# Kernel tuning notes

Measured on AMD Instinct MI355X. Metric: run time of the kernel, lower is better.

Reference implementation:

```python
import jax, jax.numpy as jnp
import numpy as np

BR = 1_000_000
D = 128


def setup_inputs() -> dict:
    key = jax.random.key(0)
    ks = jax.random.split(key, 7)
    return {
        "subject_embeddings": jax.random.normal(ks[0], (BR, D), dtype=jnp.float32),
        "object_embeddings": jax.random.normal(ks[1], (BR, D), dtype=jnp.float32),
        "Vs": jax.random.normal(ks[2], (D, D), dtype=jnp.float32) / np.sqrt(D),
        "Vo": jax.random.normal(ks[3], (D, D), dtype=jnp.float32) / np.sqrt(D),
        "Ws": jax.random.normal(ks[4], (D, D), dtype=jnp.float32) / np.sqrt(D),
        "Wo": jax.random.normal(ks[5], (D, D), dtype=jnp.float32) / np.sqrt(D),
        "w": jax.random.normal(ks[6], (D,), dtype=jnp.float32),
    }


def reference(subject_embeddings, object_embeddings, Vs, Vo, Ws, Wo, w):
    s, o = subject_embeddings, object_embeddings
    # nn.Linear(x) == x @ W.T (no bias)
    gate = jax.nn.sigmoid(s @ Vs.T + o @ Vo.T)               # [Br, d]
    dot_ow = jnp.sum(o * w[None, :], axis=1, keepdims=True)  # [Br, 1]
    interaction = s * dot_ow                                  # [Br, d]
    direction = jax.nn.relu(s @ Ws.T + o @ Wo.T + interaction)
    return gate * direction
```

## Files before the change

### kernel.cpp

```cpp
#include <hip/hip_runtime.h>
#include <hip/hip_bf16.h>

#define BR_N     1000000
#define DIM      128
#define TILE_M   64
#define NTILES   (BR_N / TILE_M)
#define NTHREADS 512
#define NBLOCKS  1024

typedef __attribute__((ext_vector_type(8))) short    bf16x8;
typedef __attribute__((ext_vector_type(4))) float    f32x4;
typedef __attribute__((ext_vector_type(4))) unsigned u32x4;

static __device__ __forceinline__ unsigned pk2(float a, float b) {
    union { __hip_bfloat162 h; unsigned u; } v;
    v.h = __float22bfloat162_rn(float2{a, b});
    return v.u;
}

union FragU { bf16x8 v; u32x4 u; };

static __device__ __forceinline__ bf16x8 cvt8(const f32x4 a, const f32x4 b) {
    FragU r;
    r.u.x = pk2(a.x, a.y);
    r.u.y = pk2(a.z, a.w);
    r.u.z = pk2(b.x, b.y);
    r.u.w = pk2(b.z, b.w);
    return r.v;
}

static __device__ __forceinline__ float bf2f(unsigned short b) {
    union { unsigned u; float f; } v;
    v.u = ((unsigned)b) << 16;
    return v.f;
}

__global__ __launch_bounds__(NTHREADS, 2)
void relup_kernel(const float* __restrict__ S, const float* __restrict__ O,
                  const float* __restrict__ Vs, const float* __restrict__ Vo,
                  const float* __restrict__ Ws, const float* __restrict__ Wo,
                  const float* __restrict__ W1, float* __restrict__ out)
{
    __shared__ __align__(16) unsigned char sT[TILE_M * 256];
    __shared__ __align__(16) unsigned char oT[TILE_M * 256];
    __shared__ float dotv[TILE_M];

    const int tid  = threadIdx.x;
    const int lane = tid & 63;
    const int wv   = tid >> 6;
    const int c0   = wv << 4;

    bf16x8 fVs[4], fVo[4], fWs[4], fWo[4];
    {
        const int wr = c0 + (lane & 15);
        const int wc = (lane >> 4) << 3;
        #pragma unroll
        for (int kk = 0; kk < 4; ++kk) {
            const int off = wr * DIM + kk * 32 + wc;
            fVs[kk] = cvt8(*(const f32x4*)(Vs + off), *(const f32x4*)(Vs + off + 4));
            fVo[kk] = cvt8(*(const f32x4*)(Vo + off), *(const f32x4*)(Vo + off + 4));
            fWs[kk] = cvt8(*(const f32x4*)(Ws + off), *(const f32x4*)(Ws + off + 4));
            fWo[kk] = cvt8(*(const f32x4*)(Wo + off), *(const f32x4*)(Wo + off + 4));
        }
    }

    const int str = tid >> 3;
    const int seg = tid & 7;
    const int swS = (str & 7) << 4;
    const int sb0 = str * 256 + ((seg * 32) ^ swS);
    const int sb1 = str * 256 + (((seg * 32) + 16) ^ swS);
    const float* wp = W1 + seg * 16;

    int t = blockIdx.x;

    f32x4 Ps0, Ps1, Ps2, Ps3, Po0, Po1, Po2, Po3;
    {
        const float* sp = S + (t * TILE_M + str) * DIM + seg * 16;
        const float* op = O + (t * TILE_M + str) * DIM + seg * 16;
        Ps0 = ((const f32x4*)sp)[0]; Ps1 = ((const f32x4*)sp)[1];
        Ps2 = ((const f32x4*)sp)[2]; Ps3 = ((const f32x4*)sp)[3];
        Po0 = ((const f32x4*)op)[0]; Po1 = ((const f32x4*)op)[1];
        Po2 = ((const f32x4*)op)[2]; Po3 = ((const f32x4*)op)[3];
    }

    while (t < NTILES) {
        const int row0 = t * TILE_M;
        const int tn   = t + (int)gridDim.x;
        const int tp   = (tn < NTILES) ? tn : t;

        {
            const f32x4 w0 = ((const f32x4*)wp)[0], w1 = ((const f32x4*)wp)[1];
            const f32x4 w2 = ((const f32x4*)wp)[2], w3 = ((const f32x4*)wp)[3];
            float p = Po0.x*w0.x + Po0.y*w0.y + Po0.z*w0.z + Po0.w*w0.w
                    + Po1.x*w1.x + Po1.y*w1.y + Po1.z*w1.z + Po1.w*w1.w
                    + Po2.x*w2.x + Po2.y*w2.y + Po2.z*w2.z + Po2.w*w2.w
                    + Po3.x*w3.x + Po3.y*w3.y + Po3.z*w3.z + Po3.w*w3.w;

            u32x4 pa = { pk2(Ps0.x,Ps0.y), pk2(Ps0.z,Ps0.w), pk2(Ps1.x,Ps1.y), pk2(Ps1.z,Ps1.w) };
            u32x4 pb = { pk2(Ps2.x,Ps2.y), pk2(Ps2.z,Ps2.w), pk2(Ps3.x,Ps3.y), pk2(Ps3.z,Ps3.w) };
            u32x4 pc = { pk2(Po0.x,Po0.y), pk2(Po0.z,Po0.w), pk2(Po1.x,Po1.y), pk2(Po1.z,Po1.w) };
            u32x4 pd = { pk2(Po2.x,Po2.y), pk2(Po2.z,Po2.w), pk2(Po3.x,Po3.y), pk2(Po3.z,Po3.w) };
            *(u32x4*)(sT + sb0) = pa;
            *(u32x4*)(sT + sb1) = pb;
            *(u32x4*)(oT + sb0) = pc;
            *(u32x4*)(oT + sb1) = pd;

            {
                const float* sp = S + (tp * TILE_M + str) * DIM + seg * 16;
                const float* op = O + (tp * TILE_M + str) * DIM + seg * 16;
                Ps0 = ((const f32x4*)sp)[0]; Ps1 = ((const f32x4*)sp)[1];
                Ps2 = ((const f32x4*)sp)[2]; Ps3 = ((const f32x4*)sp)[3];
                Po0 = ((const f32x4*)op)[0]; Po1 = ((const f32x4*)op)[1];
                Po2 = ((const f32x4*)op)[2]; Po3 = ((const f32x4*)op)[3];
            }

            p += __shfl_xor(p, 1);
            p += __shfl_xor(p, 2);
            p += __shfl_xor(p, 4);
            if (seg == 0) dotv[str] = p;
        }
        __syncthreads();

        #pragma unroll
        for (int b = 0; b < 4; ++b) {
            const int r0  = b << 4;
            const int ar  = r0 + (lane & 15);
            const int swA = (ar & 7) << 4;
            const int acb = (lane >> 4) << 4;
            bf16x8 fs[4], fo[4];
            #pragma unroll
            for (int kk = 0; kk < 4; ++kk) {
                const int cb = ((kk << 6) + acb) ^ swA;
                fs[kk] = *(const bf16x8*)(sT + ar * 256 + cb);
                fo[kk] = *(const bf16x8*)(oT + ar * 256 + cb);
            }
            f32x4 accg = {0.f, 0.f, 0.f, 0.f};
            f32x4 accd = {0.f, 0.f, 0.f, 0.f};
            #pragma unroll
            for (int kk = 0; kk < 4; ++kk) {
                accg = __builtin_amdgcn_mfma_f32_16x16x32_bf16(fs[kk], fVs[kk], accg, 0, 0, 0);
                accg = __builtin_amdgcn_mfma_f32_16x16x32_bf16(fo[kk], fVo[kk], accg, 0, 0, 0);
                accd = __builtin_amdgcn_mfma_f32_16x16x32_bf16(fs[kk], fWs[kk], accd, 0, 0, 0);
                accd = __builtin_amdgcn_mfma_f32_16x16x32_bf16(fo[kk], fWo[kk], accd, 0, 0, 0);
            }
            const int col = c0 + (lane & 15);
            #pragma unroll
            for (int r = 0; r < 4; ++r) {
                const int row = r0 + ((lane >> 4) << 2) + r;
                const int gi  = (row0 + row) * DIM + col;
                const int sOff = row * 256 + ((col * 2) ^ ((row & 7) << 4));
                const float sval  = bf2f(*(const unsigned short*)(sT + sOff));
                const float inter = sval * dotv[row];
                const float gate  = 1.0f / (1.0f + __expf(-accg[r]));
                float dir = accd[r] + inter;
                dir = dir > 0.0f ? dir : 0.0f;
                out[gi] = gate * dir;
            }
        }
        __syncthreads();
        t = tn;
    }
}

extern "C" void kernel_launch(void* const* d_in, const int* in_sizes, int n_in,
                              void* d_out, int out_size, void* d_ws, size_t ws_size,
                              hipStream_t stream) {
    const float* S  = (const float*)d_in[0];
    const float* O  = (const float*)d_in[1];
    const float* Vs = (const float*)d_in[2];
    const float* Vo = (const float*)d_in[3];
    const float* Ws = (const float*)d_in[4];
    const float* Wo = (const float*)d_in[5];
    const float* w  = (const float*)d_in[6];
    float* out = (float*)d_out;
    relup_kernel<<<NBLOCKS, NTHREADS, 0, stream>>>(S, O, Vs, Vo, Ws, Wo, w, out);
}
```

Baseline: 320.8 us.

## Double-buffer LDS tiles and transpose MFMA operands for vectorized output stores

Doubles the shared-memory staging buffers so the next tile's bf16 pack, LDS store and dot-product run after the current tile's MFMA work. This removes one of the two barriers per iteration. The MFMA operand order is swapped so each lane holds four consecutive output columns of a single row, which allows one 16-byte global store per lane instead of four scalar stores. The cost is twice the LDS footprint, which may limit occupancy at two blocks per CU, and the result tile must be rebuilt in the transposed layout.

```diff
diff --git a/kernel.cpp b/kernel.cpp
--- a/kernel.cpp
+++ b/kernel.cpp
@@ -11,6 +11,7 @@
 typedef __attribute__((ext_vector_type(8))) short    bf16x8;
 typedef __attribute__((ext_vector_type(4))) float    f32x4;
 typedef __attribute__((ext_vector_type(4))) unsigned u32x4;
+typedef __attribute__((ext_vector_type(2))) unsigned u32x2;
 
 static __device__ __forceinline__ unsigned pk2(float a, float b) {
     union { __hip_bfloat162 h; unsigned u; } v;
@@ -41,9 +42,9 @@
                   const float* __restrict__ Ws, const float* __restrict__ Wo,
                   const float* __restrict__ W1, float* __restrict__ out)
 {
-    __shared__ __align__(16) unsigned char sT[TILE_M * 256];
-    __shared__ __align__(16) unsigned char oT[TILE_M * 256];
-    __shared__ float dotv[TILE_M];
+    __shared__ __align__(16) unsigned char sT[2][TILE_M * 256];
+    __shared__ __align__(16) unsigned char oT[2][TILE_M * 256];
+    __shared__ float dotv[2][TILE_M];
 
     const int tid  = threadIdx.x;
     const int lane = tid & 63;
@@ -71,7 +72,8 @@
     const int sb1 = str * 256 + (((seg * 32) + 16) ^ swS);
     const float* wp = W1 + seg * 16;
 
-    int t = blockIdx.x;
+    int t   = blockIdx.x;
+    int cur = 0;
 
     f32x4 Ps0, Ps1, Ps2, Ps3, Po0, Po1, Po2, Po3;
     {
@@ -82,45 +84,45 @@
         Po0 = ((const f32x4*)op)[0]; Po1 = ((const f32x4*)op)[1];
         Po2 = ((const f32x4*)op)[2]; Po3 = ((const f32x4*)op)[3];
     }
+    {
+        const f32x4 w0 = ((const f32x4*)wp)[0], w1 = ((const f32x4*)wp)[1];
+        const f32x4 w2 = ((const f32x4*)wp)[2], w3 = ((const f32x4*)wp)[3];
+        float p = Po0.x*w0.x + Po0.y*w0.y + Po0.z*w0.z + Po0.w*w0.w
+                + Po1.x*w1.x + Po1.y*w1.y + Po1.z*w1.z + Po1.w*w1.w
+                + Po2.x*w2.x + Po2.y*w2.y + Po2.z*w2.z + Po2.w*w2.w
+                + Po3.x*w3.x + Po3.y*w3.y + Po3.z*w3.z + Po3.w*w3.w;
+        u32x4 pa = { pk2(Ps0.x,Ps0.y), pk2(Ps0.z,Ps0.w), pk2(Ps1.x,Ps1.y), pk2(Ps1.z,Ps1.w) };
+        u32x4 pb = { pk2(Ps2.x,Ps2.y), pk2(Ps2.z,Ps2.w), pk2(Ps3.x,Ps3.y), pk2(Ps3.z,Ps3.w) };
+        u32x4 pc = { pk2(Po0.x,Po0.y), pk2(Po0.z,Po0.w), pk2(Po1.x,Po1.y), pk2(Po1.z,Po1.w) };
+        u32x4 pd = { pk2(Po2.x,Po2.y), pk2(Po2.z,Po2.w), pk2(Po3.x,Po3.y), pk2(Po3.z,Po3.w) };
+        *(u32x4*)(sT[0] + sb0) = pa;
+        *(u32x4*)(sT[0] + sb1) = pb;
+        *(u32x4*)(oT[0] + sb0) = pc;
+        *(u32x4*)(oT[0] + sb1) = pd;
+        p += __shfl_xor(p, 1);
+        p += __shfl_xor(p, 2);
+        p += __shfl_xor(p, 4);
+        if (seg == 0) dotv[0][str] = p;
+    }
+    __syncthreads();
 
     while (t < NTILES) {
         const int row0 = t * TILE_M;
         const int tn   = t + (int)gridDim.x;
         const int tp   = (tn < NTILES) ? tn : t;
+        const int nxt  = cur ^ 1;
 
         {
-            const f32x4 w0 = ((const f32x4*)wp)[0], w1 = ((const f32x4*)wp)[1];
-            const f32x4 w2 = ((const f32x4*)wp)[2], w3 = ((const f32x4*)wp)[3];
-            float p = Po0.x*w0.x + Po0.y*w0.y + Po0.z*w0.z + Po0.w*w0.w
-                    + Po1.x*w1.x + Po1.y*w1.y + Po1.z*w1.z + Po1.w*w1.w
-                    + Po2.x*w2.x + Po2.y*w2.y + Po2.z*w2.z + Po2.w*w2.w
-                    + Po3.x*w3.x + Po3.y*w3.y + Po3.z*w3.z + Po3.w*w3.w;
-
-            u32x4 pa = { pk2(Ps0.x,Ps0.y), pk2(Ps0.z,Ps0.w), pk2(Ps1.x,Ps1.y), pk2(Ps1.z,Ps1.w) };
-            u32x4 pb = { pk2(Ps2.x,Ps2.y), pk2(Ps2.z,Ps2.w), pk2(Ps3.x,Ps3.y), pk2(Ps3.z,Ps3.w) };
-            u32x4 pc = { pk2(Po0.x,Po0.y), pk2(Po0.z,Po0.w), pk2(Po1.x,Po1.y), pk2(Po1.z,Po1.w) };
-            u32x4 pd = { pk2(Po2.x,Po2.y), pk2(Po2.z,Po2.w), pk2(Po3.x,Po3.y), pk2(Po3.z,Po3.w) };
-            *(u32x4*)(sT + sb0) = pa;
-            *(u32x4*)(sT + sb1) = pb;
-            *(u32x4*)(oT + sb0) = pc;
-            *(u32x4*)(oT + sb1) = pd;
-
-            {
-                const float* sp = S + (tp * TILE_M + str) * DIM + seg * 16;
-                const float* op = O + (tp * TILE_M + str) * DIM + seg * 16;
-                Ps0 = ((const f32x4*)sp)[0]; Ps1 = ((const f32x4*)sp)[1];
-                Ps2 = ((const f32x4*)sp)[2]; Ps3 = ((const f32x4*)sp)[3];
-                Po0 = ((const f32x4*)op)[0]; Po1 = ((const f32x4*)op)[1];
-                Po2 = ((const f32x4*)op)[2]; Po3 = ((const f32x4*)op)[3];
-            }
-
-            p += __shfl_xor(p, 1);
-            p += __shfl_xor(p, 2);
-            p += __shfl_xor(p, 4);
-            if (seg == 0) dotv[str] = p;
-        }
-        __syncthreads();
-
+            const float* sp = S + (tp * TILE_M + str) * DIM + seg * 16;
+            const float* op = O + (tp * TILE_M + str) * DIM + seg * 16;
+            Ps0 = ((const f32x4*)sp)[0]; Ps1 = ((const f32x4*)sp)[1];
+            Ps2 = ((const f32x4*)sp)[2]; Ps3 = ((const f32x4*)sp)[3];
+            Po0 = ((const f32x4*)op)[0]; Po1 = ((const f32x4*)op)[1];
+            Po2 = ((const f32x4*)op)[2]; Po3 = ((const f32x4*)op)[3];
+        }
+
+        const unsigned char* sTc = sT[cur];
+        const unsigned char* oTc = oT[cur];
         #pragma unroll
         for (int b = 0; b < 4; ++b) {
             const int r0  = b << 4;
@@ -131,34 +133,65 @@
             #pragma unroll
             for (int kk = 0; kk < 4; ++kk) {
                 const int cb = ((kk << 6) + acb) ^ swA;
-                fs[kk] = *(const bf16x8*)(sT + ar * 256 + cb);
-                fo[kk] = *(const bf16x8*)(oT + ar * 256 + cb);
+                fs[kk] = *(const bf16x8*)(sTc + ar * 256 + cb);
+                fo[kk] = *(const bf16x8*)(oTc + ar * 256 + cb);
             }
             f32x4 accg = {0.f, 0.f, 0.f, 0.f};
             f32x4 accd = {0.f, 0.f, 0.f, 0.f};
             #pragma unroll
             for (int kk = 0; kk < 4; ++kk) {
-                accg = __builtin_amdgcn_mfma_f32_16x16x32_bf16(fs[kk], fVs[kk], accg, 0, 0, 0);
-                accg = __builtin_amdgcn_mfma_f32_16x16x32_bf16(fo[kk], fVo[kk], accg, 0, 0, 0);
-                accd = __builtin_amdgcn_mfma_f32_16x16x32_bf16(fs[kk], fWs[kk], accd, 0, 0, 0);
-                accd = __builtin_amdgcn_mfma_f32_16x16x32_bf16(fo[kk], fWo[kk], accd, 0, 0, 0);
+                accg = __builtin_amdgcn_mfma_f32_16x16x32_bf16(fVs[kk], fs[kk], accg, 0, 0, 0);
+                accg = __builtin_amdgcn_mfma_f32_16x16x32_bf16(fVo[kk], fo[kk], accg, 0, 0, 0);
+                accd = __builtin_amdgcn_mfma_f32_16x16x32_bf16(fWs[kk], fs[kk], accd, 0, 0, 0);
+                accd = __builtin_amdgcn_mfma_f32_16x16x32_bf16(fWo[kk], fo[kk], accd, 0, 0, 0);
             }
-            const int col = c0 + (lane & 15);
-            #pragma unroll
-            for (int r = 0; r < 4; ++r) {
-                const int row = r0 + ((lane >> 4) << 2) + r;
-                const int gi  = (row0 + row) * DIM + col;
-                const int sOff = row * 256 + ((col * 2) ^ ((row & 7) << 4));
-                const float sval  = bf2f(*(const unsigned short*)(sT + sOff));
-                const float inter = sval * dotv[row];
-                const float gate  = 1.0f / (1.0f + __expf(-accg[r]));
-                float dir = accd[r] + inter;
-                dir = dir > 0.0f ? dir : 0.0f;
-                out[gi] = gate * dir;
+            const int row = r0 + (lane & 15);
+            const int f0  = c0 + ((lane >> 4) << 2);
+            const float dv = dotv[cur][row];
+            const int sOff = row * 256 + ((2 * f0) ^ ((row & 7) << 4));
+            const u32x2 sv = *(const u32x2*)(sTc + sOff);
+            const float sq0 = bf2f((unsigned short)(sv.x & 0xffffu));
+            const float sq1 = bf2f((unsigned short)(sv.x >> 16));
+            const float sq2 = bf2f((unsigned short)(sv.y & 0xffffu));
+            const float sq3 = bf2f((unsigned short)(sv.y >> 16));
+            f32x4 res;
+            {
+                const float g0 = 1.0f / (1.0f + __expf(-accg[0]));
+                const float g1 = 1.0f / (1.0f + __expf(-accg[1]));
+                const float g2 = 1.0f / (1.0f + __expf(-accg[2]));
+                const float g3 = 1.0f / (1.0f + __expf(-accg[3]));
+                float d0 = accd[0] + sq0 * dv; d0 = d0 > 0.f ? d0 : 0.f;
+                float d1 = accd[1] + sq1 * dv; d1 = d1 > 0.f ? d1 : 0.f;
+                float d2 = accd[2] + sq2 * dv; d2 = d2 > 0.f ? d2 : 0.f;
+                float d3 = accd[3] + sq3 * dv; d3 = d3 > 0.f ? d3 : 0.f;
+                res.x = g0 * d0; res.y = g1 * d1; res.z = g2 * d2; res.w = g3 * d3;
             }
+            *(f32x4*)(out + (row0 + row) * DIM + f0) = res;
+        }
+
+        {
+            const f32x4 w0 = ((const f32x4*)wp)[0], w1 = ((const f32x4*)wp)[1];
+            const f32x4 w2 = ((const f32x4*)wp)[2], w3 = ((const f32x4*)wp)[3];
+            float p = Po0.x*w0.x + Po0.y*w0.y + Po0.z*w0.z + Po0.w*w0.w
+                    + Po1.x*w1.x + Po1.y*w1.y + Po1.z*w1.z + Po1.w*w1.w
+                    + Po2.x*w2.x + Po2.y*w2.y + Po2.z*w2.z + Po2.w*w2.w
+                    + Po3.x*w3.x + Po3.y*w3.y + Po3.z*w3.z + Po3.w*w3.w;
+            u32x4 pa = { pk2(Ps0.x,Ps0.y), pk2(Ps0.z,Ps0.w), pk2(Ps1.x,Ps1.y), pk2(Ps1.z,Ps1.w) };
+            u32x4 pb = { pk2(Ps2.x,Ps2.y), pk2(Ps2.z,Ps2.w), pk2(Ps3.x,Ps3.y), pk2(Ps3.z,Ps3.w) };
+            u32x4 pc = { pk2(Po0.x,Po0.y), pk2(Po0.z,Po0.w), pk2(Po1.x,Po1.y), pk2(Po1.z,Po1.w) };
+            u32x4 pd = { pk2(Po2.x,Po2.y), pk2(Po2.z,Po2.w), pk2(Po3.x,Po3.y), pk2(Po3.z,Po3.w) };
+            *(u32x4*)(sT[nxt] + sb0) = pa;
+            *(u32x4*)(sT[nxt] + sb1) = pb;
+            *(u32x4*)(oT[nxt] + sb0) = pc;
+            *(u32x4*)(oT[nxt] + sb1) = pd;
+            p += __shfl_xor(p, 1);
+            p += __shfl_xor(p, 2);
+            p += __shfl_xor(p, 4);
+            if (seg == 0) dotv[nxt][str] = p;
         }
         __syncthreads();
         t = tn;
+        cur = nxt;
     }
 }
 
```

New measurement: 327.0 us. No clear change (+1.9%).

## Double-buffer LDS tiles with two-deep register prefetch and vectorized transposed stores

Applied to the files above, without the earlier changes.

Makes the tile loop a software pipeline. Two LDS buffers are used, and global loads for the tile two steps ahead are issued into alternating register sets, so only one barrier per tile is needed instead of two. The MFMA operands are swapped to compute the transposed product, which lets each lane write four contiguous output columns as one 16-byte store instead of scalar strided stores. The grid is halved to 512 blocks, and the w vector is hoisted out of the loop. The cost is higher register and LDS pressure, which may reduce occupancy.

```diff
diff --git a/kernel.cpp b/kernel.cpp
--- a/kernel.cpp
+++ b/kernel.cpp
@@ -6,11 +6,13 @@
 #define TILE_M   64
 #define NTILES   (BR_N / TILE_M)
 #define NTHREADS 512
-#define NBLOCKS  1024
+#define NBLOCKS  512
+#define TBYTES   (TILE_M * 256)
 
 typedef __attribute__((ext_vector_type(8))) short    bf16x8;
 typedef __attribute__((ext_vector_type(4))) float    f32x4;
 typedef __attribute__((ext_vector_type(4))) unsigned u32x4;
+typedef __attribute__((ext_vector_type(2))) unsigned u32x2;
 
 static __device__ __forceinline__ unsigned pk2(float a, float b) {
     union { __hip_bfloat162 h; unsigned u; } v;
@@ -35,15 +37,21 @@
     return v.f;
 }
 
+static __device__ __forceinline__ void tile_barrier() {
+    asm volatile("s_waitcnt lgkmcnt(0)" ::: "memory");
+    __builtin_amdgcn_s_barrier();
+    asm volatile("" ::: "memory");
+}
+
 __global__ __launch_bounds__(NTHREADS, 2)
 void relup_kernel(const float* __restrict__ S, const float* __restrict__ O,
                   const float* __restrict__ Vs, const float* __restrict__ Vo,
                   const float* __restrict__ Ws, const float* __restrict__ Wo,
                   const float* __restrict__ W1, float* __restrict__ out)
 {
-    __shared__ __align__(16) unsigned char sT[TILE_M * 256];
-    __shared__ __align__(16) unsigned char oT[TILE_M * 256];
-    __shared__ float dotv[TILE_M];
+    __shared__ __align__(16) unsigned char sT[2][TBYTES];
+    __shared__ __align__(16) unsigned char oT[2][TBYTES];
+    __shared__ float dotv[2][TILE_M];
 
     const int tid  = threadIdx.x;
     const int lane = tid & 63;
@@ -69,97 +77,132 @@
     const int swS = (str & 7) << 4;
     const int sb0 = str * 256 + ((seg * 32) ^ swS);
     const int sb1 = str * 256 + (((seg * 32) + 16) ^ swS);
+
     const float* wp = W1 + seg * 16;
+    const f32x4 wq0 = ((const f32x4*)wp)[0], wq1 = ((const f32x4*)wp)[1];
+    const f32x4 wq2 = ((const f32x4*)wp)[2], wq3 = ((const f32x4*)wp)[3];
+
+    f32x4 As0, As1, As2, As3, Ao0, Ao1, Ao2, Ao3;
+    f32x4 Bs0, Bs1, Bs2, Bs3, Bo0, Bo1, Bo2, Bo3;
+
+#define ISSUE(tIdx, Rs0,Rs1,Rs2,Rs3, Ro0,Ro1,Ro2,Ro3) do {                 \
+        const float* sp_ = S + ((tIdx) * TILE_M + str) * DIM + seg * 16;   \
+        const float* op_ = O + ((tIdx) * TILE_M + str) * DIM + seg * 16;   \
+        Rs0 = ((const f32x4*)sp_)[0]; Rs1 = ((const f32x4*)sp_)[1];        \
+        Rs2 = ((const f32x4*)sp_)[2]; Rs3 = ((const f32x4*)sp_)[3];        \
+        Ro0 = ((const f32x4*)op_)[0]; Ro1 = ((const f32x4*)op_)[1];        \
+        Ro2 = ((const f32x4*)op_)[2]; Ro3 = ((const f32x4*)op_)[3];        \
+    } while (0)
+
+#define PACK(buf, Rs0,Rs1,Rs2,Rs3, Ro0,Ro1,Ro2,Ro3) do {                               \
+        float p_ = Ro0.x*wq0.x + Ro0.y*wq0.y + Ro0.z*wq0.z + Ro0.w*wq0.w               \
+                 + Ro1.x*wq1.x + Ro1.y*wq1.y + Ro1.z*wq1.z + Ro1.w*wq1.w               \
+                 + Ro2.x*wq2.x + Ro2.y*wq2.y + Ro2.z*wq2.z + Ro2.w*wq2.w               \
+                 + Ro3.x*wq3.x + Ro3.y*wq3.y + Ro3.z*wq3.z + Ro3.w*wq3.w;              \
+        u32x4 pa_ = { pk2(Rs0.x,Rs0.y), pk2(Rs0.z,Rs0.w), pk2(Rs1.x,Rs1.y), pk2(Rs1.z,Rs1.w) }; \
+        u32x4 pb_ = { pk2(Rs2.x,Rs2.y), pk2(Rs2.z,Rs2.w), pk2(Rs3.x,Rs3.y), pk2(Rs3.z,Rs3.w) }; \
+        u32x4 pc_ = { pk2(Ro0.x,Ro0.y), pk2(Ro0.z,Ro0.w), pk2(Ro1.x,Ro1.y), pk2(Ro1.z,Ro1.w) }; \
+        u32x4 pd_ = { pk2(Ro2.x,Ro2.y), pk2(Ro2.z,Ro2.w), pk2(Ro3.x,Ro3.y), pk2(Ro3.z,Ro3.w) }; \
+        *(u32x4*)(sT[buf] + sb0) = pa_;                                                \
+        *(u32x4*)(sT[buf] + sb1) = pb_;                                                \
+        *(u32x4*)(oT[buf] + sb0) = pc_;                                                \
+        *(u32x4*)(oT[buf] + sb1) = pd_;                                                \
+        p_ += __shfl_xor(p_, 1);                                                       \
+        p_ += __shfl_xor(p_, 2);                                                       \
+        p_ += __shfl_xor(p_, 4);                                                       \
+        if (seg == 0) dotv[buf][str] = p_;                                             \
+    } while (0)
+
+#define COMPUTE(tIdx, buf) do {                                                        \
+        const int row0_ = (tIdx) * TILE_M;                                             \
+        const unsigned char* sTc_ = sT[buf];                                           \
+        const unsigned char* oTc_ = oT[buf];                                           \
+        const float* dvc_ = dotv[buf];                                                 \
+        _Pragma("unroll")                                                              \
+        for (int b = 0; b < 4; ++b) {                                                  \
+            const int r0_  = b << 4;                                                   \
+            const int ar_  = r0_ + (lane & 15);                                        \
+            const int swA_ = (ar_ & 7) << 4;                                           \
+            const int acb_ = (lane >> 4) << 4;                                         \
+            bf16x8 fs_[4], fo_[4];                                                     \
+            _Pragma("unroll")                                                          \
+            for (int kk = 0; kk < 4; ++kk) {                                           \
+                const int cb_ = ((kk << 6) + acb_) ^ swA_;                             \
+                fs_[kk] = *(const bf16x8*)(sTc_ + ar_ * 256 + cb_);                    \
+                fo_[kk] = *(const bf16x8*)(oTc_ + ar_ * 256 + cb_);                    \
+            }                                                                          \
+            f32x4 accg_ = {0.f, 0.f, 0.f, 0.f};                                        \
+            f32x4 accd_ = {0.f, 0.f, 0.f, 0.f};                                        \
+            _Pragma("unroll")                                                          \
+            for (int kk = 0; kk < 4; ++kk) {                                           \
+                accg_ = __builtin_amdgcn_mfma_f32_16x16x32_bf16(fVs[kk], fs_[kk], accg_, 0, 0, 0); \
+                accg_ = __builtin_amdgcn_mfma_f32_16x16x32_bf16(fVo[kk], fo_[kk], accg_, 0, 0, 0); \
+                accd_ = __builtin_amdgcn_mfma_f32_16x16x32_bf16(fWs[kk], fs_[kk], accd_, 0, 0, 0); \
+                accd_ = __builtin_amdgcn_mfma_f32_16x16x32_bf16(fWo[kk], fo_[kk], accd_, 0, 0, 0); \
+            }                                                                          \
+                   \
+            const int row_ = r0_ + (lane & 15);                                        \
+            const int f0_  = c0 + ((lane >> 4) << 2);                                  \
+            const float dv_ = dvc_[row_];                                              \
+            const int sOff_ = row_ * 256 + ((2 * f0_) ^ ((row_ & 7) << 4));            \
+            const u32x2 sv_ = *(const u32x2*)(sTc_ + sOff_);                           \
+            const float sq0_ = bf2f((unsigned short)(sv_.x & 0xffffu));                \
+            const float sq1_ = bf2f((unsigned short)(sv_.x >> 16));                    \
+            const float sq2_ = bf2f((unsigned short)(sv_.y & 0xffffu));                \
+            const float sq3_ = bf2f((unsigned short)(sv_.y >> 16));                    \
+            f32x4 res_;                                                                \
+            {                                                                          \
+                const float g0_ = 1.0f / (1.0f + __expf(-accg_[0]));                   \
+                const float g1_ = 1.0f / (1.0f + __expf(-accg_[1]));                   \
+                const float g2_ = 1.0f / (1.0f + __expf(-accg_[2]));                   \
+                const float g3_ = 1.0f / (1.0f + __expf(-accg_[3]));                   \
+                float d0_ = accd_[0] + sq0_ * dv_; d0_ = d0_ > 0.f ? d0_ : 0.f;        \
+                float d1_ = accd_[1] + sq1_ * dv_; d1_ = d1_ > 0.f ? d1_ : 0.f;        \
+                float d2_ = accd_[2] + sq2_ * dv_; d2_ = d2_ > 0.f ? d2_ : 0.f;        \
+                float d3_ = accd_[3] + sq3_ * dv_; d3_ = d3_ > 0.f ? d3_ : 0.f;        \
+                res_.x = g0_ * d0_; res_.y = g1_ * d1_;                                \
+                res_.z = g2_ * d2_; res_.w = g3_ * d3_;                                \
+            }                                                                          \
+            *(f32x4*)(out + (row0_ + row_) * DIM + f0_) = res_;                        \
+        }                                                                              \
+    } while (0)
 
     int t = blockIdx.x;
 
-    f32x4 Ps0, Ps1, Ps2, Ps3, Po0, Po1, Po2, Po3;
+    ISSUE(t, As0,As1,As2,As3, Ao0,Ao1,Ao2,Ao3);
     {
-        const float* sp = S + (t * TILE_M + str) * DIM + seg * 16;
-        const float* op = O + (t * TILE_M + str) * DIM + seg * 16;
-        Ps0 = ((const f32x4*)sp)[0]; Ps1 = ((const f32x4*)sp)[1];
-        Ps2 = ((const f32x4*)sp)[2]; Ps3 = ((const f32x4*)sp)[3];
-        Po0 = ((const f32x4*)op)[0]; Po1 = ((const f32x4*)op)[1];
-        Po2 = ((const f32x4*)op)[2]; Po3 = ((const f32x4*)op)[3];
+        int tB = t + NBLOCKS; if (tB >= NTILES) tB = t;
+        ISSUE(tB, Bs0,Bs1,Bs2,Bs3, Bo0,Bo1,Bo2,Bo3);
     }
-
-    while (t < NTILES) {
-        const int row0 = t * TILE_M;
-        const int tn   = t + (int)gridDim.x;
-        const int tp   = (tn < NTILES) ? tn : t;
-
+    PACK(0, As0,As1,As2,As3, Ao0,Ao1,Ao2,Ao3);
+    tile_barrier();
+
+    int cur = 0;
+    for (;;) {
         {
-            const f32x4 w0 = ((const f32x4*)wp)[0], w1 = ((const f32x4*)wp)[1];
-            const f32x4 w2 = ((const f32x4*)wp)[2], w3 = ((const f32x4*)wp)[3];
-            float p = Po0.x*w0.x + Po0.y*w0.y + Po0.z*w0.z + Po0.w*w0.w
-                    + Po1.x*w1.x + Po1.y*w1.y + Po1.z*w1.z + Po1.w*w1.w
-                    + Po2.x*w2.x + Po2.y*w2.y + Po2.z*w2.z + Po2.w*w2.w
-                    + Po3.x*w3.x + Po3.y*w3.y + Po3.z*w3.z + Po3.w*w3.w;
-
-            u32x4 pa = { pk2(Ps0.x,Ps0.y), pk2(Ps0.z,Ps0.w), pk2(Ps1.x,Ps1.y), pk2(Ps1.z,Ps1.w) };
-            u32x4 pb = { pk2(Ps2.x,Ps2.y), pk2(Ps2.z,Ps2.w), pk2(Ps3.x,Ps3.y), pk2(Ps3.z,Ps3.w) };
-            u32x4 pc = { pk2(Po0.x,Po0.y), pk2(Po0.z,Po0.w), pk2(Po1.x,Po1.y), pk2(Po1.z,Po1.w) };
-            u32x4 pd = { pk2(Po2.x,Po2.y), pk2(Po2.z,Po2.w), pk2(Po3.x,Po3.y), pk2(Po3.z,Po3.w) };
-            *(u32x4*)(sT + sb0) = pa;
-            *(u32x4*)(sT + sb1) = pb;
-            *(u32x4*)(oT + sb0) = pc;
-            *(u32x4*)(oT + sb1) = pd;
-
-            {
-                const float* sp = S + (tp * TILE_M + str) * DIM + seg * 16;
-                const float* op = O + (tp * TILE_M + str) * DIM + seg * 16;
-                Ps0 = ((const f32x4*)sp)[0]; Ps1 = ((const f32x4*)sp)[1];
-                Ps2 = ((const f32x4*)sp)[2]; Ps3 = ((const f32x4*)sp)[3];
-                Po0 = ((const f32x4*)op)[0]; Po1 = ((const f32x4*)op)[1];
-                Po2 = ((const f32x4*)op)[2]; Po3 = ((const f32x4*)op)[3];
-            }
-
-            p += __shfl_xor(p, 1);
-            p += __shfl_xor(p, 2);
-            p += __shfl_xor(p, 4);
-            if (seg == 0) dotv[str] = p;
+            const bool more1 = (t + NBLOCKS)     < NTILES;
+            const bool more2 = (t + 2 * NBLOCKS) < NTILES;
+            if (more2) ISSUE(t + 2 * NBLOCKS, As0,As1,As2,As3, Ao0,Ao1,Ao2,Ao3);
+            COMPUTE(t, cur);
+            if (!more1) break;
+            PACK(cur ^ 1, Bs0,Bs1,Bs2,Bs3, Bo0,Bo1,Bo2,Bo3);
+            tile_barrier();
+            cur ^= 1; t += NBLOCKS;
         }
-        __syncthreads();
-
-        #pragma unroll
-        for (int b = 0; b < 4; ++b) {
-            const int r0  = b << 4;
-            const int ar  = r0 + (lane & 15);
-            const int swA = (ar & 7) << 4;
-            const int acb = (lane >> 4) << 4;
-            bf16x8 fs[4], fo[4];
-            #pragma unroll
-            for (int kk = 0; kk < 4; ++kk) {
-                const int cb = ((kk << 6) + acb) ^ swA;
-                fs[kk] = *(const bf16x8*)(sT + ar * 256 + cb);
-                fo[kk] = *(const bf16x8*)(oT + ar * 256 + cb);
-            }
-            f32x4 accg = {0.f, 0.f, 0.f, 0.f};
-            f32x4 accd = {0.f, 0.f, 0.f, 0.f};
-            #pragma unroll
-            for (int kk = 0; kk < 4; ++kk) {
-                accg = __builtin_amdgcn_mfma_f32_16x16x32_bf16(fs[kk], fVs[kk], accg, 0, 0, 0);
-                accg = __builtin_amdgcn_mfma_f32_16x16x32_bf16(fo[kk], fVo[kk], accg, 0, 0, 0);
-                accd = __builtin_amdgcn_mfma_f32_16x16x32_bf16(fs[kk], fWs[kk], accd, 0, 0, 0);
-                accd = __builtin_amdgcn_mfma_f32_16x16x32_bf16(fo[kk], fWo[kk], accd, 0, 0, 0);
-            }
-            const int col = c0 + (lane & 15);
-            #pragma unroll
-            for (int r = 0; r < 4; ++r) {
-                const int row = r0 + ((lane >> 4) << 2) + r;
-                const int gi  = (row0 + row) * DIM + col;
-                const int sOff = row * 256 + ((col * 2) ^ ((row & 7) << 4));
-                const float sval  = bf2f(*(const unsigned short*)(sT + sOff));
-                const float inter = sval * dotv[row];
-                const float gate  = 1.0f / (1.0f + __expf(-accg[r]));
-                float dir = accd[r] + inter;
-                dir = dir > 0.0f ? dir : 0.0f;
-                out[gi] = gate * dir;
-            }
+        {
+            const bool more1 = (t + NBLOCKS)     < NTILES;
+            const bool more2 = (t + 2 * NBLOCKS) < NTILES;
+            if (more2) ISSUE(t + 2 * NBLOCKS, Bs0,Bs1,Bs2,Bs3, Bo0,Bo1,Bo2,Bo3);
+            COMPUTE(t, cur);
+            if (!more1) break;
+            PACK(cur ^ 1, As0,As1,As2,As3, Ao0,Ao1,Ao2,Ao3);
+            tile_barrier();
+            cur ^= 1; t += NBLOCKS;
         }
-        __syncthreads();
-        t = tn;
     }
+#undef ISSUE
+#undef PACK
+#undef COMPUTE
 }
 
 extern "C" void kernel_launch(void* const* d_in, const int* in_sizes, int n_in,
```

Measured after the change: 304.4 us, median of 2. -5.1%, faster.
